# Performance work log

Hardware: AMD Instinct MI355X
Metric: run time of the kernel (lower is better)

Reference implementation:

```python
import jax, jax.numpy as jnp
import numpy as np

N_EMBD = 1024
N_HEAD = 16
LN_EPS = 1e-5


def layernorm(x, w, eps=LN_EPS):
    mu = jnp.mean(x, axis=-1, keepdims=True)
    var = jnp.mean(jnp.square(x - mu), axis=-1, keepdims=True)
    return (x - mu) * jax.lax.rsqrt(var + eps) * w


def setup_inputs() -> dict:
    key = jax.random.key(0)
    ks = jax.random.split(key, 6)
    B, T, C, F = 4, 2048, N_EMBD, 4 * N_EMBD
    s = 0.02
    return {
        "x": jax.random.normal(ks[0], (B, T, C), jnp.float32),
        "ln1_w": jnp.ones((C,), jnp.float32),
        "w_attn": jax.random.normal(ks[1], (C, 3 * C), jnp.float32) * s,
        "w_proj": jax.random.normal(ks[2], (C, C), jnp.float32) * s,
        "ln2_w": jnp.ones((C,), jnp.float32),
        "w_fc1": jax.random.normal(ks[3], (C, F), jnp.float32) * s,
        "b_fc1": jnp.zeros((F,), jnp.float32),
        "w_fc2": jax.random.normal(ks[4], (F, C), jnp.float32) * s,
        "b_fc2": jnp.zeros((C,), jnp.float32),
    }


def reference(x, ln1_w, w_attn, w_proj, ln2_w, w_fc1, b_fc1, w_fc2, b_fc2):
    B, T, C = x.shape
    H = N_HEAD
    D = C // H
    # --- attention sub-block (dropout = 0, eval mode) ---
    h = layernorm(x, ln1_w)
    qkv = h @ w_attn  # [B, T, 3C]
    q, k, v = jnp.split(qkv, 3, axis=-1)
    q = q.reshape(B, T, H, D)
    k = k.reshape(B, T, H, D)
    v = v.reshape(B, T, H, D)
    scale = 1.0 / np.sqrt(D).astype(np.float32)
    att = jnp.einsum("bqhd,bkhd->bhqk", q, k) * scale  # [B, H, T, T]
    causal = jnp.tril(jnp.ones((T, T), bool))
    att = jnp.where(causal, att, -jnp.inf)
    att = jax.nn.softmax(att, axis=-1)
    y = jnp.einsum("bhqk,bkhd->bqhd", att, v).reshape(B, T, C)
    x = x + y @ w_proj
    # --- MLP sub-block ---
    h = layernorm(x, ln2_w)
    h = jax.nn.relu(h @ w_fc1 + b_fc1)
    x = x + (h @ w_fc2 + b_fc2)
    return x
```

## Files before the change

kernel.cpp:

```cpp
#include <hip/hip_runtime.h>
#include <cstdint>


#define CDIM 1024
#define TSEQ 2048
#define NBATCH 4
#define NHEAD 16
#define HDIM 64
#define FDIM 4096

typedef unsigned short u16;
typedef __attribute__((ext_vector_type(8))) short s16x8;
typedef __attribute__((ext_vector_type(4))) float f32x4;

__device__ __forceinline__ u16 f2bu(float f) {
    uint32_t u = __builtin_bit_cast(uint32_t, f);
    uint32_t r = (u + 0x7FFFu + ((u >> 16) & 1u)) >> 16;
    return (u16)r;
}

__device__ __forceinline__ uint32_t cvtpk(float lo, float hi) {
    uint32_t r;
    asm("v_cvt_pk_bf16_f32 %0, %1, %2" : "=v"(r) : "v"(lo), "v"(hi));
    return r;
}

typedef __attribute__((address_space(3))) unsigned int lds_u32;
typedef __attribute__((address_space(1))) const unsigned int glb_u32;
__device__ __forceinline__ void gload_lds16(const void* g, void* l) {
    __builtin_amdgcn_global_load_lds((glb_u32*)g, (lds_u32*)l, 16, 0, 0);
}

#define FENCE() asm volatile("" ::: "memory")

__global__ __launch_bounds__(256) void twb_k(const float* __restrict__ in,
                                             u16* __restrict__ out, int K, int N) {
    __shared__ float tile[32][33];
    int n0 = blockIdx.x * 32, k0 = blockIdx.y * 32;
    int tx = threadIdx.x & 31, ty = threadIdx.x >> 5;
#pragma unroll
    for (int i = 0; i < 32; i += 8)
        tile[ty + i][tx] = in[(size_t)(k0 + ty + i) * N + n0 + tx];
    __syncthreads();
#pragma unroll
    for (int i = 0; i < 32; i += 8)
        out[(size_t)(n0 + ty + i) * K + k0 + tx] = f2bu(tile[tx][ty + i]);
}

__global__ __launch_bounds__(256) void ln_k(const float* __restrict__ x,
                                            const float* __restrict__ w,
                                            u16* __restrict__ out) {
    int row = blockIdx.x;
    int t = threadIdx.x;
    const float4* xr = (const float4*)(x + (size_t)row * CDIM);
    float4 v = xr[t];
    float s = v.x + v.y + v.z + v.w;
    float sq = v.x * v.x + v.y * v.y + v.z * v.z + v.w * v.w;
#pragma unroll
    for (int o = 32; o > 0; o >>= 1) { s += __shfl_xor(s, o); sq += __shfl_xor(sq, o); }
    __shared__ float ps[4], pq[4];
    int wid = t >> 6, lane = t & 63;
    if (lane == 0) { ps[wid] = s; pq[wid] = sq; }
    __syncthreads();
    s = ps[0] + ps[1] + ps[2] + ps[3];
    sq = pq[0] + pq[1] + pq[2] + pq[3];
    float mu = s * (1.0f / CDIM);
    float var = sq * (1.0f / CDIM) - mu * mu;
    float rstd = rsqrtf(var + 1e-5f);
    float4 wv = ((const float4*)w)[t];
    union { u16 h[4]; uint2 u; } pk;
    pk.h[0] = f2bu((v.x - mu) * rstd * wv.x);
    pk.h[1] = f2bu((v.y - mu) * rstd * wv.y);
    pk.h[2] = f2bu((v.z - mu) * rstd * wv.z);
    pk.h[3] = f2bu((v.w - mu) * rstd * wv.w);
    ((uint2*)(out + (size_t)row * CDIM))[t] = pk.u;
}

template <int EPI>
__global__ __launch_bounds__(512, 2) void gemm8p(const u16* __restrict__ A,
                                                 const u16* __restrict__ Bt,
                                                 void* __restrict__ Cout,
                                                 u16* __restrict__ Vout,
                                                 const float* __restrict__ bias,
                                                 int M, int N, int K) {
    __shared__ __align__(16) u16 L[2][2][2][128][64];
    const int tid = threadIdx.x, lane = tid & 63, wid = tid >> 6;
    const int lr = lane & 15, lk = lane >> 4;
    const int wr = wid >> 2, wcn = wid & 3;
    const int nbx = gridDim.x;
    const int nwg = nbx * gridDim.y;
    const int bid = blockIdx.y * nbx + blockIdx.x;
    const int swz = (bid & 7) * (nwg >> 3) + (bid >> 3);
    const int m0 = (swz / nbx) * 256, n0 = (swz % nbx) * 256;
    const int NT = K >> 6;

    auto STG = [&](int kt, int part, int kh) {
        const u16* src = part ? Bt : A;
        const int base0 = part ? n0 : m0;
        u16* dst = &L[kt & 1][part][kh][0][0];
#pragma unroll
        for (int i = 0; i < 2; ++i) {
            int t = i * 512 + tid;
            int r2 = t >> 3, se = t & 7;
            int s = se ^ (r2 & 7);
            int row = 2 * r2 + (s >> 2), c = s & 3;
            gload_lds16(src + (size_t)(base0 + row) * K + kt * 64 + kh * 32 + c * 8,
                        dst + (size_t)(i * 512 + wid * 64) * 8);
        }
    };

    f32x4 acc[8][4];
#pragma unroll
    for (int i = 0; i < 8; ++i)
#pragma unroll
        for (int j = 0; j < 4; ++j) acc[i][j] = (f32x4){0.f, 0.f, 0.f, 0.f};

    STG(0, 0, 0); STG(0, 1, 0); STG(0, 0, 1); STG(0, 1, 1);
    STG(1, 0, 0); STG(1, 1, 0);
    asm volatile("s_waitcnt vmcnt(8)" ::: "memory");
    FENCE(); __builtin_amdgcn_s_barrier(); FENCE();

    const int se = (((lr & 1) << 2) | lk) ^ (lr >> 1);
    const int rA0 = wr * 64 + (lr >> 1);
    const int rB0 = wcn * 32 + (lr >> 1);

    s16x8 af[4], bf[4];

#define LDA(kh, ch) \
    { _Pragma("unroll") for (int q = 0; q < 4; ++q) \
        af[q] = *(const s16x8*)&L[slot][0][kh][rA0 + (ch) * 32 + q * 8][se * 8]; }
#define LDB(kh) \
    { _Pragma("unroll") for (int q = 0; q < 4; ++q) \
        bf[q] = *(const s16x8*)&L[slot][1][kh][rB0 + q * 8][se * 8]; }
#define MM(ch) \
    { __builtin_amdgcn_s_setprio(1); \
      _Pragma("unroll") for (int qm = 0; qm < 4; ++qm) \
      _Pragma("unroll") for (int ni = 0; ni < 4; ++ni) \
        acc[(ch) * 4 + qm][ni] = __builtin_amdgcn_mfma_f32_16x16x32_bf16( \
            af[qm], bf[ni], acc[(ch) * 4 + qm][ni], 0, 0, 0); \
      __builtin_amdgcn_s_setprio(0); }
#define BAR() { FENCE(); __builtin_amdgcn_s_barrier(); FENCE(); }
#define CKPT() asm volatile("s_waitcnt vmcnt(8)" ::: "memory")

    for (int j = 0; j < NT; ++j) {
        const int slot = j & 1;
        const int jn1 = (j + 1 < NT) ? j + 1 : j + 1 - NT;
        const int jn2 = (j + 2 < NT) ? j + 2 : j + 2 - NT;
        LDA(0, 0); LDB(0);
        STG(jn1, 0, 1);
        BAR(); MM(0); BAR();
        LDA(0, 1);
        STG(jn1, 1, 1);
        CKPT();
        BAR(); MM(1); BAR();
        LDA(1, 0); LDB(1);
        STG(jn2, 0, 0);
        BAR(); MM(0); BAR();
        LDA(1, 1);
        STG(jn2, 1, 0);
        CKPT();
        BAR(); MM(1); BAR();
    }
#undef LDA
#undef LDB
#undef MM
#undef BAR
#undef CKPT

#pragma unroll
    for (int mi = 0; mi < 8; ++mi) {
#pragma unroll
        for (int ni = 0; ni < 4; ++ni) {
            int col = n0 + wcn * 64 + ni * 16 + lr;
#pragma unroll
            for (int r = 0; r < 4; ++r) {
                int row = m0 + wr * 128 + mi * 16 + lk * 4 + r;
                float v = acc[mi][ni][r];
                size_t idx = (size_t)row * N + col;
                if constexpr (EPI == 0) {
                    if (col < 2048) {
                        ((u16*)Cout)[idx] = f2bu(v);
                    } else {
                        int bb = row >> 11, tt = row & 2047, cc = col - 2048;
                        Vout[((size_t)(bb * 16 + (cc >> 6)) * 64 + (cc & 63)) * 2048 + tt] = f2bu(v);
                    }
                } else {
                    ((u16*)Cout)[idx] = f2bu(fmaxf(v + bias[col], 0.f));
                }
            }
        }
    }
}

template <int EPI>
__global__ __launch_bounds__(256) void gemm_bt(const u16* __restrict__ A,
                                               const u16* __restrict__ Bt,
                                               void* __restrict__ Cout,
                                               const float* __restrict__ bias,
                                               const float* __restrict__ res,
                                               int M, int N, int K) {
    __shared__ u16 Al[128 * 32];
    __shared__ u16 Bl[128 * 32];
    int tid = threadIdx.x;
    int lane = tid & 63, wid = tid >> 6;
    int wr = wid >> 1, wc = wid & 1;
    int lr = lane & 15, lk = lane >> 4;
    const int nbx = gridDim.x;
    const int nwg = nbx * gridDim.y;
    const int bid = blockIdx.y * nbx + blockIdx.x;
    const int swz = (bid & 7) * (nwg >> 3) + (bid >> 3);
    int m0 = (swz / nbx) * 128, n0 = (swz % nbx) * 128;

    f32x4 acc[4][4];
#pragma unroll
    for (int i = 0; i < 4; ++i)
#pragma unroll
        for (int j = 0; j < 4; ++j) acc[i][j] = (f32x4){0.f, 0.f, 0.f, 0.f};

    for (int k0 = 0; k0 < K; k0 += 32) {
        __syncthreads();
#pragma unroll
        for (int i = 0; i < 2; ++i) {
            int cb = (wid * 2 + i) * 64;
            int c = cb + lane;
            int r = c >> 2, kc = c & 3;
            gload_lds16(A + (size_t)(m0 + r) * K + k0 + kc * 8, Al + cb * 8);
            gload_lds16(Bt + (size_t)(n0 + r) * K + k0 + kc * 8, Bl + cb * 8);
        }
        __syncthreads();
        s16x8 af[4], bfr[4];
#pragma unroll
        for (int mi = 0; mi < 4; ++mi)
            af[mi] = *(const s16x8*)(Al + (wr * 64 + mi * 16 + lr) * 32 + lk * 8);
#pragma unroll
        for (int ni = 0; ni < 4; ++ni)
            bfr[ni] = *(const s16x8*)(Bl + (wc * 64 + ni * 16 + lr) * 32 + lk * 8);
#pragma unroll
        for (int mi = 0; mi < 4; ++mi)
#pragma unroll
            for (int ni = 0; ni < 4; ++ni)
                acc[mi][ni] = __builtin_amdgcn_mfma_f32_16x16x32_bf16(
                    af[mi], bfr[ni], acc[mi][ni], 0, 0, 0);
    }

#pragma unroll
    for (int mi = 0; mi < 4; ++mi) {
#pragma unroll
        for (int ni = 0; ni < 4; ++ni) {
            int col = n0 + wc * 64 + ni * 16 + lr;
#pragma unroll
            for (int r = 0; r < 4; ++r) {
                int row = m0 + wr * 64 + mi * 16 + lk * 4 + r;
                float v = acc[mi][ni][r];
                size_t idx = (size_t)row * N + col;
                if constexpr (EPI == 1) {
                    ((float*)Cout)[idx] = res[idx] + v;
                } else {
                    ((float*)Cout)[idx] = res[idx] + v + bias[col];
                }
            }
        }
    }
}

__global__ __launch_bounds__(256) void attn_k(const u16* __restrict__ qkv,
                                              const u16* __restrict__ vT,
                                              u16* __restrict__ y) {
    int pidx = blockIdx.x;
    int bh = blockIdx.y;
    int b = bh >> 4, h = bh & 15;
    int tid = threadIdx.x, lane = tid & 63, wid = tid >> 6;
    int lr = lane & 15, lk = lane >> 4;

    __shared__ u16 Kl[2][8192];
    __shared__ u16 Vl[2][8192];
    __shared__ __align__(16) u16 Pl[4][2048];

    const u16* qkp = qkv + (size_t)(b * TSEQ) * 3072 + h * HDIM;
    const u16* kkp = qkp + CDIM;
    const u16* vtp = vT + (size_t)bh * HDIM * TSEQ;

    auto STAGE = [&](int buf, int kv0) {
#pragma unroll
        for (int c = 0; c < 4; ++c) {
            int s = c * 256 + wid * 64 + lane;
            int kr = s >> 3, kc = s & 7;
            int gkc = kc ^ (kr & 7);
            gload_lds16(kkp + (size_t)(kv0 + kr) * 3072 + gkc * 8,
                        &Kl[buf][(size_t)(c * 256 + wid * 64) * 8]);
            int vd = s >> 4, vc = s & 15;
            int gvc = (vc & 8) | ((vc ^ vd) & 7);
            gload_lds16(vtp + (size_t)vd * TSEQ + kv0 + gvc * 8,
                        &Vl[buf][(size_t)(c * 256 + wid * 64) * 8]);
        }
    };

    auto qtile = [&](int qt) {
        int qbase = qt * 128 + wid * 32;
        int qend = qbase + 31;
        s16x8 qf[2][2];
#pragma unroll
        for (int qs = 0; qs < 2; ++qs)
#pragma unroll
            for (int db = 0; db < 2; ++db)
                qf[qs][db] = *(const s16x8*)(qkp +
                    (size_t)(qbase + qs * 16 + lr) * 3072 + db * 32 + lk * 8);
        f32x4 acc[2][4];
#pragma unroll
        for (int qs = 0; qs < 2; ++qs)
#pragma unroll
            for (int ds = 0; ds < 4; ++ds) acc[qs][ds] = (f32x4){0.f, 0.f, 0.f, 0.f};
        float mrun[2] = {-1e30f, -1e30f};
        float lrun[2] = {0.f, 0.f};

        int nt = qt + 1;
        STAGE(0, 0);
        for (int t = 0; t < nt; ++t) {
            int cur = t & 1;
            int kv0 = t * 128;
            if (t + 1 < nt) {
                STAGE(cur ^ 1, (t + 1) * 128);
                asm volatile("s_waitcnt vmcnt(8)" ::: "memory");
            } else {
                asm volatile("s_waitcnt vmcnt(0)" ::: "memory");
            }
            __builtin_amdgcn_s_barrier();
            FENCE();

            const u16* Kb = &Kl[cur][0];
            const u16* Vb = &Vl[cur][0];

            f32x4 st[8][2];
#pragma unroll
            for (int ks = 0; ks < 8; ++ks)
#pragma unroll
                for (int qs = 0; qs < 2; ++qs)
                    st[ks][qs] = (f32x4){-1e30f, -1e30f, -1e30f, -1e30f};
            __builtin_amdgcn_s_setprio(1);
#pragma unroll
            for (int ks = 0; ks < 8; ++ks) {
                if (kv0 + ks * 16 <= qend) {
                    s16x8 kf0 = *(const s16x8*)(Kb + (ks * 16 + lr) * 64 + ((lk ^ (lr & 7)) * 8));
                    s16x8 kf1 = *(const s16x8*)(Kb + (ks * 16 + lr) * 64 + (((4 + lk) ^ (lr & 7)) * 8));
#pragma unroll
                    for (int qs = 0; qs < 2; ++qs) {
                        f32x4 z = (f32x4){0.f, 0.f, 0.f, 0.f};
                        z = __builtin_amdgcn_mfma_f32_16x16x32_bf16(kf0, qf[qs][0], z, 0, 0, 0);
                        st[ks][qs] = __builtin_amdgcn_mfma_f32_16x16x32_bf16(kf1, qf[qs][1], z, 0, 0, 0);
                    }
                }
            }
            __builtin_amdgcn_s_setprio(0);

            if (kv0 + 127 > qbase) {
#pragma unroll
                for (int ks = 0; ks < 8; ++ks)
#pragma unroll
                    for (int qs = 0; qs < 2; ++qs)
#pragma unroll
                        for (int r = 0; r < 4; ++r) {
                            int k = kv0 + ks * 16 + lk * 4 + r;
                            int q = qbase + qs * 16 + lr;
                            if (k > q) st[ks][qs][r] = -1e30f;
                        }
            }

#pragma unroll
            for (int qs = 0; qs < 2; ++qs) {
                float pmax = -1e30f;
#pragma unroll
                for (int ks = 0; ks < 8; ++ks) {
                    float a = fmaxf(fmaxf(st[ks][qs][0], st[ks][qs][1]),
                                    fmaxf(st[ks][qs][2], st[ks][qs][3]));
                    pmax = fmaxf(pmax, a);
                }
                pmax = fmaxf(pmax, __shfl_xor(pmax, 16));
                pmax = fmaxf(pmax, __shfl_xor(pmax, 32));
                float mnew = fmaxf(mrun[qs], pmax);
                float scale = __expf((mrun[qs] - mnew) * 0.125f);
                mrun[qs] = mnew;
                float psum = 0.f;
#pragma unroll
                for (int ks = 0; ks < 8; ++ks) {
#pragma unroll
                    for (int r = 0; r < 4; ++r) {
                        float pv = __expf((st[ks][qs][r] - mnew) * 0.125f);
                        st[ks][qs][r] = pv;
                        psum += pv;
                    }
                }
                psum += __shfl_xor(psum, 16);
                psum += __shfl_xor(psum, 32);
                lrun[qs] = lrun[qs] * scale + psum;
#pragma unroll
                for (int ds = 0; ds < 4; ++ds)
#pragma unroll
                    for (int r = 0; r < 4; ++r) acc[qs][ds][r] *= scale;
            }

#pragma unroll
            for (int hh = 0; hh < 2; ++hh) {
                if (kv0 + hh * 64 > qend) break;
#pragma unroll
                for (int qs = 0; qs < 2; ++qs)
#pragma unroll
                    for (int ksp = 0; ksp < 4; ++ksp) {
                        int ks = hh * 4 + ksp;
                        uint32_t w0 = cvtpk(st[ks][qs][0], st[ks][qs][1]);
                        uint32_t w1 = cvtpk(st[ks][qs][2], st[ks][qs][3]);
                        int q = qs * 16 + lr;
                        int cp = (2 * ksp + (lk >> 1)) ^ (lr & 7);
                        *(uint2*)&Pl[wid][q * 64 + cp * 8 + (lk & 1) * 4] =
                            make_uint2(w0, w1);
                    }
#pragma unroll
                for (int khp = 0; khp < 2; ++khp) {
                    int kh = hh * 2 + khp;
                    if (kv0 + kh * 32 > qend) break;
                    s16x8 vtf[4];
#pragma unroll
                    for (int ds = 0; ds < 4; ++ds) {
                        int ch = kh * 4 + lk;
                        int chs = (ch & 8) | ((ch ^ (lr & 7)) & 7);
                        vtf[ds] = *(const s16x8*)(Vb + (ds * 16 + lr) * 128 + chs * 8);
                    }
                    s16x8 pa[2];
#pragma unroll
                    for (int qs = 0; qs < 2; ++qs) {
                        int q = qs * 16 + lr;
                        int cp = (4 * khp + lk) ^ (lr & 7);
                        pa[qs] = *(const s16x8*)&Pl[wid][q * 64 + cp * 8];
                    }
                    __builtin_amdgcn_s_setprio(1);
#pragma unroll
                    for (int qs = 0; qs < 2; ++qs)
#pragma unroll
                        for (int ds = 0; ds < 4; ++ds)
                            acc[qs][ds] = __builtin_amdgcn_mfma_f32_16x16x32_bf16(
                                vtf[ds], pa[qs], acc[qs][ds], 0, 0, 0);
                    __builtin_amdgcn_s_setprio(0);
                }
            }
            FENCE();
            __builtin_amdgcn_s_barrier();
            FENCE();
        }

        float rl[2] = {1.f / lrun[0], 1.f / lrun[1]};
#pragma unroll
        for (int qs = 0; qs < 2; ++qs) {
            int q = qbase + qs * 16 + lr;
            u16* yr = y + (size_t)(b * TSEQ + q) * CDIM + h * HDIM;
#pragma unroll
            for (int ds = 0; ds < 4; ++ds)
#pragma unroll
                for (int r = 0; r < 4; ++r)
                    yr[ds * 16 + lk * 4 + r] = f2bu(acc[qs][ds][r] * rl[qs]);
        }
    };

    qtile(pidx);
    qtile(15 - pidx);
}

extern "C" void kernel_launch(void* const* d_in, const int* in_sizes, int n_in,
                              void* d_out, int out_size, void* d_ws, size_t ws_size,
                              hipStream_t stream) {
    (void)in_sizes; (void)n_in; (void)out_size; (void)ws_size;
    const float* x      = (const float*)d_in[0];
    const float* ln1_w  = (const float*)d_in[1];
    const float* w_attn = (const float*)d_in[2];
    const float* w_proj = (const float*)d_in[3];
    const float* ln2_w  = (const float*)d_in[4];
    const float* w_fc1  = (const float*)d_in[5];
    const float* b_fc1  = (const float*)d_in[6];
    const float* w_fc2  = (const float*)d_in[7];
    const float* b_fc2  = (const float*)d_in[8];
    float* out = (float*)d_out;
    char* ws = (char*)d_ws;

    u16*   wT_attn = (u16*)(ws + 0);
    u16*   wT_proj = (u16*)(ws + 6291456);
    u16*   wT_fc1  = (u16*)(ws + 8388608);
    u16*   wT_fc2  = (u16*)(ws + 16777216);
    u16*   h       = (u16*)(ws + 25165824);
    u16*   qkvb    = (u16*)(ws + 41943040);
    u16*   yb      = (u16*)(ws + 92274688);
    float* x1      = (float*)(ws + 109051904);
    u16*   vTb     = (u16*)(ws + 109051904);
    u16*   h3      = (u16*)(ws + 41943040);

    twb_k<<<dim3(3072 / 32, 1024 / 32), 256, 0, stream>>>(w_attn, wT_attn, 1024, 3072);
    twb_k<<<dim3(1024 / 32, 1024 / 32), 256, 0, stream>>>(w_proj, wT_proj, 1024, 1024);
    twb_k<<<dim3(4096 / 32, 1024 / 32), 256, 0, stream>>>(w_fc1, wT_fc1, 1024, 4096);
    twb_k<<<dim3(1024 / 32, 4096 / 32), 256, 0, stream>>>(w_fc2, wT_fc2, 4096, 1024);

    ln_k<<<8192, 256, 0, stream>>>(x, ln1_w, h);
    gemm8p<0><<<dim3(3072 / 256, 8192 / 256), 512, 0, stream>>>(h, wT_attn, qkvb, vTb, nullptr, 8192, 3072, 1024);
    attn_k<<<dim3(8, NBATCH * NHEAD), 256, 0, stream>>>(qkvb, vTb, yb);
    gemm_bt<1><<<dim3(1024 / 128, 8192 / 128), 256, 0, stream>>>(yb, wT_proj, x1, nullptr, x, 8192, 1024, 1024);
    ln_k<<<8192, 256, 0, stream>>>(x1, ln2_w, h);
    gemm8p<2><<<dim3(4096 / 256, 8192 / 256), 512, 0, stream>>>(h, wT_fc1, h3, nullptr, b_fc1, 8192, 4096, 1024);
    gemm_bt<3><<<dim3(1024 / 128, 8192 / 128), 256, 0, stream>>>(h3, wT_fc2, out, b_fc2, x1, 8192, 1024, 4096);
}
```

Measured before the change: 591.1 us.

## Read K and V tiles directly from global memory in attention kernel

Removes the double-buffered LDS staging of K and V tiles along with its per-iteration barriers and waitcnts. Each wave now loads its K and V MFMA fragments directly from global memory and relies on L1/L2 caching for the reuse across the four waves. This cuts LDS usage, which may raise occupancy, and removes block-wide synchronisation. The cost is redundant global traffic and exposed load latency, since there is no longer a prefetch overlapping the next tile with compute.

```diff
diff --git a/kernel.cpp b/kernel.cpp
--- a/kernel.cpp
+++ b/kernel.cpp
@@ -272,28 +272,11 @@
     int tid = threadIdx.x, lane = tid & 63, wid = tid >> 6;
     int lr = lane & 15, lk = lane >> 4;
 
-    __shared__ u16 Kl[2][8192];
-    __shared__ u16 Vl[2][8192];
     __shared__ __align__(16) u16 Pl[4][2048];
 
     const u16* qkp = qkv + (size_t)(b * TSEQ) * 3072 + h * HDIM;
     const u16* kkp = qkp + CDIM;
     const u16* vtp = vT + (size_t)bh * HDIM * TSEQ;
-
-    auto STAGE = [&](int buf, int kv0) {
-#pragma unroll
-        for (int c = 0; c < 4; ++c) {
-            int s = c * 256 + wid * 64 + lane;
-            int kr = s >> 3, kc = s & 7;
-            int gkc = kc ^ (kr & 7);
-            gload_lds16(kkp + (size_t)(kv0 + kr) * 3072 + gkc * 8,
-                        &Kl[buf][(size_t)(c * 256 + wid * 64) * 8]);
-            int vd = s >> 4, vc = s & 15;
-            int gvc = (vc & 8) | ((vc ^ vd) & 7);
-            gload_lds16(vtp + (size_t)vd * TSEQ + kv0 + gvc * 8,
-                        &Vl[buf][(size_t)(c * 256 + wid * 64) * 8]);
-        }
-    };
 
     auto qtile = [&](int qt) {
         int qbase = qt * 128 + wid * 32;
@@ -314,21 +297,8 @@
         float lrun[2] = {0.f, 0.f};
 
         int nt = qt + 1;
-        STAGE(0, 0);
         for (int t = 0; t < nt; ++t) {
-            int cur = t & 1;
             int kv0 = t * 128;
-            if (t + 1 < nt) {
-                STAGE(cur ^ 1, (t + 1) * 128);
-                asm volatile("s_waitcnt vmcnt(8)" ::: "memory");
-            } else {
-                asm volatile("s_waitcnt vmcnt(0)" ::: "memory");
-            }
-            __builtin_amdgcn_s_barrier();
-            FENCE();
-
-            const u16* Kb = &Kl[cur][0];
-            const u16* Vb = &Vl[cur][0];
 
             f32x4 st[8][2];
 #pragma unroll
@@ -336,21 +306,22 @@
 #pragma unroll
                 for (int qs = 0; qs < 2; ++qs)
                     st[ks][qs] = (f32x4){-1e30f, -1e30f, -1e30f, -1e30f};
-            __builtin_amdgcn_s_setprio(1);
 #pragma unroll
             for (int ks = 0; ks < 8; ++ks) {
                 if (kv0 + ks * 16 <= qend) {
-                    s16x8 kf0 = *(const s16x8*)(Kb + (ks * 16 + lr) * 64 + ((lk ^ (lr & 7)) * 8));
-                    s16x8 kf1 = *(const s16x8*)(Kb + (ks * 16 + lr) * 64 + (((4 + lk) ^ (lr & 7)) * 8));
+                    const u16* krow = kkp + (size_t)(kv0 + ks * 16 + lr) * 3072;
+                    s16x8 kf0 = *(const s16x8*)(krow + lk * 8);
+                    s16x8 kf1 = *(const s16x8*)(krow + 32 + lk * 8);
+                    __builtin_amdgcn_s_setprio(1);
 #pragma unroll
                     for (int qs = 0; qs < 2; ++qs) {
                         f32x4 z = (f32x4){0.f, 0.f, 0.f, 0.f};
                         z = __builtin_amdgcn_mfma_f32_16x16x32_bf16(kf0, qf[qs][0], z, 0, 0, 0);
                         st[ks][qs] = __builtin_amdgcn_mfma_f32_16x16x32_bf16(kf1, qf[qs][1], z, 0, 0, 0);
                     }
-                }
-            }
-            __builtin_amdgcn_s_setprio(0);
+                    __builtin_amdgcn_s_setprio(0);
+                }
+            }
 
             if (kv0 + 127 > qbase) {
 #pragma unroll
@@ -419,11 +390,9 @@
                     if (kv0 + kh * 32 > qend) break;
                     s16x8 vtf[4];
 #pragma unroll
-                    for (int ds = 0; ds < 4; ++ds) {
-                        int ch = kh * 4 + lk;
-                        int chs = (ch & 8) | ((ch ^ (lr & 7)) & 7);
-                        vtf[ds] = *(const s16x8*)(Vb + (ds * 16 + lr) * 128 + chs * 8);
-                    }
+                    for (int ds = 0; ds < 4; ++ds)
+                        vtf[ds] = *(const s16x8*)(vtp +
+                            (size_t)(ds * 16 + lr) * TSEQ + kv0 + kh * 32 + lk * 8);
                     s16x8 pa[2];
 #pragma unroll
                     for (int qs = 0; qs < 2; ++qs) {
@@ -441,9 +410,6 @@
                     __builtin_amdgcn_s_setprio(0);
                 }
             }
-            FENCE();
-            __builtin_amdgcn_s_barrier();
-            FENCE();
         }
 
         float rl[2] = {1.f / lrun[0], 1.f / lrun[1]};
```

Result: faster. 578.2 us (-2.2%).
